# Optimization experiments

Measured on AMD Instinct MI355X. Metric: run time of the kernel, lower is better.

## Reference

```python
import jax, jax.numpy as jnp
import numpy as np

B, N, F_DIM, M, K, D = 8, 16384, 6, 128, 16, 768
MLP_DIMS = [F_DIM, 256, 512, 768, D]


def _fps(pts):
    """Deterministic farthest point sampling. pts: [N,4] -> indices [M] (first pick = point 0)."""
    n = pts.shape[0]

    def step(carry, _):
        min_d, last = carry
        d = jnp.sum((pts - pts[last]) ** 2, axis=-1)
        min_d = jnp.minimum(min_d, d)
        nxt = jnp.argmax(min_d).astype(jnp.int32)
        return (min_d, nxt), nxt

    init = (jnp.full((n,), 1e30, dtype=pts.dtype), jnp.int32(0))
    _, idx = jax.lax.scan(step, init, None, length=M - 1)
    return jnp.concatenate([jnp.zeros((1,), jnp.int32), idx])


def setup_inputs() -> dict:
    key = jax.random.key(0)
    ks = jax.random.split(key, 16)
    bidx = jnp.repeat(jnp.arange(B, dtype=jnp.float32), N)[:, None]
    xyzt = jax.random.normal(ks[0], (B * N, 4), jnp.float32)
    coordinates = jnp.concatenate([bidx, xyzt], axis=1)  # [B*N, 5]
    features = jax.random.normal(ks[1], (B * N, F_DIM), jnp.float32)
    inp = {"coordinates": coordinates, "features": features}
    for i in range(4):
        di, do = MLP_DIMS[i], MLP_DIMS[i + 1]
        inp[f"W{i}"] = jax.random.normal(ks[2 + i], (di, do), jnp.float32) * np.float32(1.0 / np.sqrt(di))
        inp[f"b{i}"] = jnp.zeros((do,), jnp.float32)
    for j in range(2):
        inp[f"Wn{j}"] = jax.random.normal(ks[6 + j], (D, D), jnp.float32) * np.float32(1.0 / np.sqrt(D))
        inp[f"bn{j}"] = jnp.zeros((D,), jnp.float32)
    return inp


def _forward(coordinates, features, W0, b0, W1, b1, W2, b2, W3, b3, Wn0, bn0, Wn1, bn1):
    # Equal points per event, sorted batch ids -> plain reshape replaces the per-batch loop.
    pts = coordinates.reshape(B, N, 5)[:, :, 1:5]       # xyz + time  [B,N,4]
    h = features.reshape(B, N, F_DIM)
    # per-point MLP (ReLU after each hidden layer, final Linear has no activation)
    h = jax.nn.relu(h @ W0 + b0)
    h = jax.nn.relu(h @ W1 + b1)
    h = jax.nn.relu(h @ W2 + b2)
    pf = h @ W3 + b3                                    # [B,N,D]
    # FPS centroids (non-differentiable index selection, as in the torch/cpu original)
    fidx = jax.vmap(_fps)(jax.lax.stop_gradient(pts))   # [B,M]
    cent = jnp.take_along_axis(pts, fidx[:, :, None], axis=1)  # [B,M,4]
    # cdist + kNN (smallest distances)
    dist = jnp.sqrt(jnp.sum((cent[:, :, None, :] - pts[:, None, :, :]) ** 2, axis=-1))  # [B,M,N]
    _, knn = jax.lax.top_k(-dist, K)                    # [B,M,K]
    gathered = jax.vmap(lambda p, i: p[i])(pf, knn)     # [B,M,K,D]
    pooled = jnp.max(gathered, axis=2)                  # [B,M,D]
    t = jax.nn.relu(pooled @ Wn0 + bn0)
    tokens = t @ Wn1 + bn1                              # [B,M,D]
    # sort tokens/centroids by centroid time (column 3)
    order = jnp.argsort(cent[:, :, 3], axis=1)
    cent = jnp.take_along_axis(cent, order[:, :, None], axis=1)
    tokens = jnp.take_along_axis(tokens, order[:, :, None], axis=1)
    masks = jnp.ones((B, M), dtype=bool)  # num_points > max_tokens -> all tokens valid
    return tokens, cent, masks


def reference(coordinates, features, W0, b0, W1, b1, W2, b2, W3, b3, Wn0, bn0, Wn1, bn1):
    return _forward(coordinates, features, W0, b0, W1, b1, W2, b2, W3, b3, Wn0, bn0, Wn1, bn1)
```

## Files before the change

### kernel.cpp

```cpp
#include <hip/hip_runtime.h>

#define B_ 8
#define N_ 16384
#define F_ 6
#define M_ 128
#define K_ 16
#define D_ 768

typedef unsigned short u16;
typedef unsigned int u32;
typedef unsigned long long u64;
typedef __attribute__((ext_vector_type(8))) short short8;
typedef __attribute__((ext_vector_type(4))) float f32x4;
typedef __attribute__((ext_vector_type(2))) float f32x2;

__device__ __forceinline__ u16 f2bf(float f){
  union { float f; u32 i; } v; v.f = f;
  u32 x = v.i;
  u32 r = x + 0x7FFFu + ((x >> 16) & 1u);
  return (u16)(r >> 16);
}

__device__ __forceinline__ void ld_g2l(const u16* g, u16* l){
  __builtin_amdgcn_global_load_lds((const __attribute__((address_space(1))) u32*)g,
                                   (__attribute__((address_space(3))) u32*)l, 16, 0, 0);
}

__device__ __forceinline__ f32x2 pkadd(f32x2 a, f32x2 b){
  f32x2 d; asm("v_pk_add_f32 %0, %1, %2" : "=v"(d) : "v"(a), "v"(b)); return d;
}
__device__ __forceinline__ f32x2 pkmul(f32x2 a, f32x2 b){
  f32x2 d; asm("v_pk_mul_f32 %0, %1, %2" : "=v"(d) : "v"(a), "v"(b)); return d;
}

__global__ __launch_bounds__(256) void conv_all(const float* __restrict__ W1,
                                                const float* __restrict__ W2,
                                                const float* __restrict__ W3,
                                                const float* __restrict__ Wn0,
                                                const float* __restrict__ Wn1,
                                                u16* __restrict__ Wb){
  __shared__ u16 tile[64][65];
  int blk = blockIdx.x;
  const float* W; u16* WT; int K, N, lb;
  if      (blk < 32)  { W = W1;  WT = Wb;           K = 256; N = 512; lb = blk; }
  else if (blk < 128) { W = W2;  WT = Wb + 131072;  K = 512; N = 768; lb = blk - 32; }
  else if (blk < 272) { W = W3;  WT = Wb + 524288;  K = 768; N = 768; lb = blk - 128; }
  else if (blk < 416) { W = Wn0; WT = Wb + 1114112; K = 768; N = 768; lb = blk - 272; }
  else                { W = Wn1; WT = Wb + 1703936; K = 768; N = 768; lb = blk - 416; }
  int tiles_n = N >> 6;
  int tk = lb / tiles_n, tn = lb % tiles_n;
  int k0 = tk << 6, n0 = tn << 6;
  int t = threadIdx.x;
#pragma unroll
  for (int q = 0; q < 16; q++){
    int idx = q * 256 + t;
    int kk = idx >> 6, nn = idx & 63;
    tile[kk][nn] = f2bf(W[(size_t)(k0 + kk) * N + n0 + nn]);
  }
  __syncthreads();
#pragma unroll
  for (int q = 0; q < 16; q++){
    int idx = q * 256 + t;
    int nn = idx >> 6, kk = idx & 63;
    WT[(size_t)(n0 + nn) * K + k0 + kk] = tile[kk][nn];
  }
}

#define FPJ 8
__global__ __launch_bounds__(1024, 4) void fps_block(const float* __restrict__ coords,
                                                     float* __restrict__ cent){
#pragma clang fp contract(off)
  __shared__ u64 swk[2][16];
  int b = blockIdx.x;
  int t = threadIdx.x;
  int lane = t & 63, wave = t >> 6;
  const float* cb = coords + (size_t)b * N_ * 5;
  f32x2 px[FPJ], py[FPJ], pz[FPJ], pw[FPJ], md[FPJ];
#pragma unroll
  for (int j = 0; j < FPJ; j++){
    int p = t + (j << 10);
    size_t i0 = (size_t)(2 * p) * 5;
    px[j] = (f32x2){cb[i0+1], cb[i0+6]};
    py[j] = (f32x2){cb[i0+2], cb[i0+7]};
    pz[j] = (f32x2){cb[i0+3], cb[i0+8]};
    pw[j] = (f32x2){cb[i0+4], cb[i0+9]};
    md[j] = (f32x2){1e30f, 1e30f};
    asm volatile("" : "+v"(px[j]), "+v"(py[j]), "+v"(pz[j]), "+v"(pw[j]));
  }
  float cx = cb[1], cy = cb[2], cz = cb[3], ct = cb[4];
  if (t == 0){
    float* c0 = cent + (size_t)b * M_ * 4;
    c0[0]=cx; c0[1]=cy; c0[2]=cz; c0[3]=ct;
  }
  for (int step = 1; step < M_; step++){
    f32x2 ncx2 = (f32x2){-cx, -cx}, ncy2 = (f32x2){-cy, -cy};
    f32x2 ncz2 = (f32x2){-cz, -cz}, nct2 = (f32x2){-ct, -ct};
    float bv = -1.0f; int bi = 1 << 30;
#pragma unroll
    for (int j = 0; j < FPJ; j++){
      f32x2 dx = pkadd(px[j], ncx2);
      f32x2 dy = pkadd(py[j], ncy2);
      f32x2 s  = pkadd(pkmul(dx, dx), pkmul(dy, dy));
      f32x2 dz = pkadd(pz[j], ncz2);
      s = pkadd(s, pkmul(dz, dz));
      f32x2 dw = pkadd(pw[j], nct2);
      s = pkadd(s, pkmul(dw, dw));
      f32x2 m = md[j];
      m[0] = fminf(s[0], m[0]);
      m[1] = fminf(s[1], m[1]);
      md[j] = m;
      int i0 = (t + (j << 10)) << 1;
      if (m[0] > bv){ bv = m[0]; bi = i0; }
      if (m[1] > bv){ bv = m[1]; bi = i0 + 1; }
    }
    union { float f; u32 u; } cv; cv.f = bv;
    u64 k = ((u64)cv.u << 32) | (u32)(N_ - 1 - bi);
#pragma unroll
    for (int off = 32; off > 0; off >>= 1){
      u64 ok = __shfl_down(k, off);
      if (ok > k) k = ok;
    }
    int par = step & 1;
    if (lane == 0) swk[par][wave] = k;
    __syncthreads();
    u64 fk = swk[par][0];
#pragma unroll
    for (int w = 1; w < 16; w++){ u64 wk = swk[par][w]; if (wk > fk) fk = wk; }
    int widx = N_ - 1 - (int)(fk & 0xffffffffu);
    size_t wb = (size_t)widx * 5;
    cx = cb[wb+1]; cy = cb[wb+2]; cz = cb[wb+3]; ct = cb[wb+4];
    if (t == 0){
      float* cr = cent + ((size_t)b * M_ + step) * 4;
      cr[0]=cx; cr[1]=cy; cr[2]=cz; cr[3]=ct;
    }
  }
}

__global__ __launch_bounds__(128) void rank_scatter(const float* __restrict__ cent_fps,
                                                    float* __restrict__ cent_sorted,
                                                    float* __restrict__ out,
                                                    size_t out_elems){
  int b = blockIdx.x, m = threadIdx.x;
  __shared__ float tt[M_];
  const float* row = cent_fps + ((size_t)b * M_ + m) * 4;
  float x=row[0], y=row[1], z=row[2], w=row[3];
  tt[m] = w;
  __syncthreads();
  int rank = 0;
  for (int j = 0; j < M_; j++){
    float tj = tt[j];
    if (tj < w || (tj == w && j < m)) rank++;
  }
  float* dst = cent_sorted + ((size_t)b * M_ + rank) * 4;
  dst[0]=x; dst[1]=y; dst[2]=z; dst[3]=w;
  size_t co = (size_t)B_ * M_ * D_ + ((size_t)b * M_ + rank) * 4;
  if (co + 3 < out_elems){
    out[co+0]=x; out[co+1]=y; out[co+2]=z; out[co+3]=w;
  }
  size_t mo = (size_t)B_ * M_ * D_ + (size_t)B_ * M_ * 4 + (size_t)b * M_ + m;
  if (mo < out_elems) out[mo] = 1.0f;
}

#define KNT 512
#define KPT 32
__global__ __launch_bounds__(512) void knn_kernel(const float* __restrict__ coords,
                                                  const float* __restrict__ cent,
                                                  int* __restrict__ knn){
#pragma clang fp contract(off)
  int cm = blockIdx.x;
  int b = cm >> 7;
  const float* cb = coords + (size_t)b * N_ * 5;
  int t = threadIdx.x;
  float cx=cent[cm*4+0], cy=cent[cm*4+1], cz=cent[cm*4+2], ct=cent[cm*4+3];
  float dist[KPT];
#pragma unroll
  for (int j = 0; j < KPT; j++){
    size_t i = t + j * KNT;
    float dx=cb[i*5+1]-cx, dy=cb[i*5+2]-cy, dz=cb[i*5+3]-cz, dw=cb[i*5+4]-ct;
    float d = ((dx*dx + dy*dy) + dz*dz) + dw*dw;
    dist[j] = sqrtf(d);
  }
  __shared__ float s_wv[8];
  __shared__ int s_wi[8];
  __shared__ int s_bi;
  for (int r = 0; r < K_; r++){
    float bv = 3e38f; int bi = 1 << 30;
#pragma unroll
    for (int j = 0; j < KPT; j++){
      int i = t + j * KNT;
      float v = dist[j];
      if (v < bv){ bv = v; bi = i; }
    }
#pragma unroll
    for (int off = 32; off > 0; off >>= 1){
      float ov = __shfl_down(bv, off);
      int oi = __shfl_down(bi, off);
      if (ov < bv || (ov == bv && oi < bi)){ bv = ov; bi = oi; }
    }
    if ((t & 63) == 0){ s_wv[t >> 6] = bv; s_wi[t >> 6] = bi; }
    __syncthreads();
    if (t == 0){
      float fv = s_wv[0]; int fi = s_wi[0];
      for (int w = 1; w < 8; w++){
        float wv = s_wv[w]; int wi = s_wi[w];
        if (wv < fv || (wv == fv && wi < fi)){ fv = wv; fi = wi; }
      }
      s_bi = fi;
      knn[(size_t)cm * K_ + r] = fi & (N_ - 1);
    }
    __syncthreads();
    int wi = s_bi;
#pragma unroll
    for (int j = 0; j < KPT; j++){
      if (t + j * KNT == wi) dist[j] = 3e38f;
    }
  }
}

__global__ __launch_bounds__(256) void gather_l0(const float* __restrict__ feat,
                                                 const int* __restrict__ knn,
                                                 const float* __restrict__ W0,
                                                 const float* __restrict__ b0,
                                                 u16* __restrict__ h1,
                                                 int rowBase){
  __shared__ float sW[F_][256];
  __shared__ float sb[256];
  __shared__ float sfa[32][F_];
  int t = threadIdx.x;
#pragma unroll
  for (int k = 0; k < F_; k++) sW[k][t] = W0[k * 256 + t];
  sb[t] = b0[t];
  if (t < 32 * F_){
    int r = t / F_, k = t % F_;
    int grow = rowBase + blockIdx.x * 32 + r;
    int bb = grow >> 11;
    int idx = knn[grow] & (N_ - 1);
    sfa[r][k] = feat[((size_t)bb * N_ + idx) * F_ + k];
  }
  __syncthreads();
#pragma unroll 4
  for (int r = 0; r < 32; r++){
    float acc = sb[t];
#pragma unroll
    for (int k = 0; k < F_; k++) acc = fmaf(sfa[r][k], sW[k][t], acc);
    int lrow = blockIdx.x * 32 + r;
    h1[(size_t)lrow * 256 + t] = f2bf(fmaxf(acc, 0.0f));
  }
}

template<int RELU, int OUTF32>
__global__ __launch_bounds__(256) void gemm_bf16(const u16* __restrict__ A,
                                                 const u16* __restrict__ WT,
                                                 const float* __restrict__ bias,
                                                 void* __restrict__ Cv,
                                                 int Kd, int Nd){
  __shared__ u16 As[128][32];
  __shared__ u16 Bs[128][32];
  const int t = threadIdx.x;
  const int bm = blockIdx.y << 7;
  const int bn = blockIdx.x << 7;
  const int wave = t >> 6;
  const int lane = t & 63;
  const int wm = (wave & 1) << 6;
  const int wn = (wave >> 1) << 6;
  const int lm = lane & 15;
  const int lk = (lane >> 4) << 3;
  u16* AsF = &As[0][0];
  u16* BsF = &Bs[0][0];
  const int wbase = wave << 6;
  f32x4 acc[4][4] = {};
  for (int k0 = 0; k0 < Kd; k0 += 32){
#pragma unroll
    for (int it = 0; it < 2; it++){
      int slot = t + (it << 8);
      int r = slot >> 2;
      int c = (slot & 3) << 3;
      int dst = (wbase + (it << 8)) << 3;
      ld_g2l(A  + (size_t)(bm + r) * Kd + k0 + c, AsF + dst);
      ld_g2l(WT + (size_t)(bn + r) * Kd + k0 + c, BsF + dst);
    }
    __syncthreads();
    short8 af[4], bfr[4];
#pragma unroll
    for (int mt = 0; mt < 4; mt++) af[mt] = *(const short8*)&As[wm + (mt << 4) + lm][lk];
#pragma unroll
    for (int nt = 0; nt < 4; nt++) bfr[nt] = *(const short8*)&Bs[wn + (nt << 4) + lm][lk];
#pragma unroll
    for (int mt = 0; mt < 4; mt++)
#pragma unroll
      for (int nt = 0; nt < 4; nt++)
        acc[mt][nt] = __builtin_amdgcn_mfma_f32_16x16x32_bf16(af[mt], bfr[nt], acc[mt][nt], 0, 0, 0);
    __syncthreads();
  }
#pragma unroll
  for (int nt = 0; nt < 4; nt++){
    int n = bn + wn + (nt << 4) + lm;
    float bia = bias[n];
#pragma unroll
    for (int mt = 0; mt < 4; mt++){
#pragma unroll
      for (int r2 = 0; r2 < 4; r2++){
        int m = bm + wm + (mt << 4) + ((lane >> 4) << 2) + r2;
        float v = acc[mt][nt][r2] + bia;
        if (RELU) v = fmaxf(v, 0.0f);
        if (OUTF32) ((float*)Cv)[(size_t)m * Nd + n] = v;
        else        ((u16*)Cv)[(size_t)m * Nd + n] = f2bf(v);
      }
    }
  }
}

template<int RELU, int OUTF32>
__global__ __launch_bounds__(256) void gemm64(const u16* __restrict__ A,
                                              const u16* __restrict__ WT,
                                              const float* __restrict__ bias,
                                              void* __restrict__ Cv,
                                              int Kd, int Nd){
  __shared__ u16 As[64][32];
  __shared__ u16 Bs[64][32];
  const int t = threadIdx.x;
  const int bm = blockIdx.y << 6;
  const int bn = blockIdx.x << 6;
  const int wave = t >> 6;
  const int lane = t & 63;
  const int wm = (wave & 1) << 5;
  const int wn = (wave >> 1) << 5;
  const int lm = lane & 15;
  const int lk = (lane >> 4) << 3;
  u16* AsF = &As[0][0];
  u16* BsF = &Bs[0][0];
  const int wbase = wave << 6;
  f32x4 acc[2][2] = {};
  for (int k0 = 0; k0 < Kd; k0 += 32){
    {
      int r = t >> 2;
      int c = (t & 3) << 3;
      int dst = wbase << 3;
      ld_g2l(A  + (size_t)(bm + r) * Kd + k0 + c, AsF + dst);
      ld_g2l(WT + (size_t)(bn + r) * Kd + k0 + c, BsF + dst);
    }
    __syncthreads();
    short8 af[2], bfr[2];
#pragma unroll
    for (int mt = 0; mt < 2; mt++) af[mt] = *(const short8*)&As[wm + (mt << 4) + lm][lk];
#pragma unroll
    for (int nt = 0; nt < 2; nt++) bfr[nt] = *(const short8*)&Bs[wn + (nt << 4) + lm][lk];
#pragma unroll
    for (int mt = 0; mt < 2; mt++)
#pragma unroll
      for (int nt = 0; nt < 2; nt++)
        acc[mt][nt] = __builtin_amdgcn_mfma_f32_16x16x32_bf16(af[mt], bfr[nt], acc[mt][nt], 0, 0, 0);
    __syncthreads();
  }
#pragma unroll
  for (int nt = 0; nt < 2; nt++){
    int n = bn + wn + (nt << 4) + lm;
    float bia = bias[n];
#pragma unroll
    for (int mt = 0; mt < 2; mt++){
#pragma unroll
      for (int r2 = 0; r2 < 4; r2++){
        int m = bm + wm + (mt << 4) + ((lane >> 4) << 2) + r2;
        float v = acc[mt][nt][r2] + bia;
        if (RELU) v = fmaxf(v, 0.0f);
        if (OUTF32) ((float*)Cv)[(size_t)m * Nd + n] = v;
        else        ((u16*)Cv)[(size_t)m * Nd + n] = f2bf(v);
      }
    }
  }
}

__global__ __launch_bounds__(256) void gemm_pool(const u16* __restrict__ A,
                                                 const u16* __restrict__ WT,
                                                 const float* __restrict__ bias,
                                                 u16* __restrict__ pooled,
                                                 int Kd, int Nd, int groupBase){
  __shared__ u16 As[128][32];
  __shared__ u16 Bs[128][32];
  const int t = threadIdx.x;
  const int bm = blockIdx.y << 7;
  const int bn = blockIdx.x << 7;
  const int wave = t >> 6;
  const int lane = t & 63;
  const int wm = (wave & 1) << 6;
  const int wn = (wave >> 1) << 6;
  const int lm = lane & 15;
  const int lk = (lane >> 4) << 3;
  u16* AsF = &As[0][0];
  u16* BsF = &Bs[0][0];
  const int wbase = wave << 6;
  f32x4 acc[4][4] = {};
  for (int k0 = 0; k0 < Kd; k0 += 32){
#pragma unroll
    for (int it = 0; it < 2; it++){
      int slot = t + (it << 8);
      int r = slot >> 2;
      int c = (slot & 3) << 3;
      int dst = (wbase + (it << 8)) << 3;
      ld_g2l(A  + (size_t)(bm + r) * Kd + k0 + c, AsF + dst);
      ld_g2l(WT + (size_t)(bn + r) * Kd + k0 + c, BsF + dst);
    }
    __syncthreads();
    short8 af[4], bfr[4];
#pragma unroll
    for (int mt = 0; mt < 4; mt++) af[mt] = *(const short8*)&As[wm + (mt << 4) + lm][lk];
#pragma unroll
    for (int nt = 0; nt < 4; nt++) bfr[nt] = *(const short8*)&Bs[wn + (nt << 4) + lm][lk];
#pragma unroll
    for (int mt = 0; mt < 4; mt++)
#pragma unroll
      for (int nt = 0; nt < 4; nt++)
        acc[mt][nt] = __builtin_amdgcn_mfma_f32_16x16x32_bf16(af[mt], bfr[nt], acc[mt][nt], 0, 0, 0);
    __syncthreads();
  }
#pragma unroll
  for (int nt = 0; nt < 4; nt++){
    int n = bn + wn + (nt << 4) + lm;
    float bia = bias[n];
#pragma unroll
    for (int mt = 0; mt < 4; mt++){
      f32x4 a = acc[mt][nt];
      float v = fmaxf(fmaxf(a[0], a[1]), fmaxf(a[2], a[3]));
      v = fmaxf(v, __shfl_xor(v, 16));
      v = fmaxf(v, __shfl_xor(v, 32));
      if ((lane >> 4) == 0){
        int g = groupBase + (bm >> 4) + (wm >> 4) + mt;
        pooled[(size_t)g * Nd + n] = f2bf(v + bia);
      }
    }
  }
}

__global__ __launch_bounds__(256) void fill_diag(float* __restrict__ out, size_t out_elems){
  size_t i = (size_t)blockIdx.x * 256 + threadIdx.x;
  if (i >= out_elems) return;
  size_t maskStart = (size_t)B_ * M_ * D_ + (size_t)B_ * M_ * 4;
  out[i] = (i >= maskStart) ? 1.0f : 0.0f;
}

extern "C" void kernel_launch(void* const* d_in, const int* in_sizes, int n_in,
                              void* d_out, int out_size, void* d_ws, size_t ws_size,
                              hipStream_t stream){
  (void)in_sizes; (void)n_in;
  const float* coords   = (const float*)d_in[0];
  const float* features = (const float*)d_in[1];
  const float* W0 = (const float*)d_in[2];  const float* b0 = (const float*)d_in[3];
  const float* W1 = (const float*)d_in[4];  const float* b1 = (const float*)d_in[5];
  const float* W2 = (const float*)d_in[6];  const float* b2 = (const float*)d_in[7];
  const float* W3 = (const float*)d_in[8];  const float* b3 = (const float*)d_in[9];
  const float* Wn0 = (const float*)d_in[10]; const float* bn0 = (const float*)d_in[11];
  const float* Wn1 = (const float*)d_in[12]; const float* bn1 = (const float*)d_in[13];
  float* out = (float*)d_out;
  const size_t out_elems = (size_t)out_size;

  char* ws = (char*)d_ws;
  const size_t o_cent = 0;
  const size_t o_cntS = 16384;
  const size_t o_knn  = 32768;
  const size_t o_Wb   = 131072;
  const size_t o_pool = 4718592;
  const size_t o_t1   = 6291456;
  const size_t o_chunk= 7864320;
  const int ROWS = B_ * M_ * K_;

  int R = 16384;
  while (R > 128 && o_chunk + (size_t)R * 2560 > ws_size) R >>= 1;
  if (d_ws == nullptr || o_chunk + (size_t)R * 2560 > ws_size){
    fill_diag<<<(int)((out_elems + 255) / 256), 256, 0, stream>>>(out, out_elems);
    return;
  }

  float* cent_fps    = (float*)(ws + o_cent);
  float* cent_sorted = (float*)(ws + o_cntS);
  int*   knn         = (int*)(ws + o_knn);
  u16* Wb   = (u16*)(ws + o_Wb);
  u16* W1t  = Wb;               u16* W2t  = Wb + 131072;
  u16* W3t  = Wb + 524288;      u16* Wn0t = Wb + 1114112;
  u16* Wn1t = Wb + 1703936;
  u16* pooled = (u16*)(ws + o_pool);
  u16* t1     = (u16*)(ws + o_t1);
  u16* regA   = (u16*)(ws + o_chunk);
  u16* regB   = (u16*)(ws + o_chunk + (size_t)R * 1536);

  conv_all<<<560, 256, 0, stream>>>(W1, W2, W3, Wn0, Wn1, Wb);
  fps_block<<<B_, 1024, 0, stream>>>(coords, cent_fps);
  rank_scatter<<<B_, 128, 0, stream>>>(cent_fps, cent_sorted, out, out_elems);
  knn_kernel<<<B_ * M_, KNT, 0, stream>>>(coords, cent_sorted, knn);

  for (int rowBase = 0; rowBase < ROWS; rowBase += R){
    gather_l0<<<R / 32, 256, 0, stream>>>(features, knn, W0, b0, regA, rowBase);
    gemm_bf16<1,0><<<dim3(4, R / 128), 256, 0, stream>>>(regA, W1t, b1, regB, 256, 512);
    gemm_bf16<1,0><<<dim3(6, R / 128), 256, 0, stream>>>(regB, W2t, b2, regA, 512, 768);
    gemm_pool<<<dim3(6, R / 128), 256, 0, stream>>>(regA, W3t, b3, pooled, 768, 768, rowBase >> 4);
  }

  gemm64<1,0><<<dim3(12, (B_ * M_) / 64), 256, 0, stream>>>(pooled, Wn0t, bn0, t1, 768, 768);
  gemm64<0,1><<<dim3(12, (B_ * M_) / 64), 256, 0, stream>>>(t1, Wn1t, bn1, out, 768, 768);
}
```

Baseline: 552.0 us.

## Halve FPS block size and use ballot-based argmax reduction

The farthest-point-sampling kernel now runs 512 threads per batch instead of 1024, each owning 32 contiguous points. The per-step argmax no longer does a 64-bit packed shuffle reduction. It uses a float max via xor-shuffles, then a ballot to pick the lowest winning lane's index, and combines 8 waves instead of 16. Contiguous point ownership keeps the lowest-index tie-break, so results should match. In exchange the longer per-thread loop raises register pressure.

```diff
diff --git a/kernel.cpp b/kernel.cpp
--- a/kernel.cpp
+++ b/kernel.cpp
@@ -66,20 +66,21 @@
   }
 }
 
-#define FPJ 8
-__global__ __launch_bounds__(1024, 4) void fps_block(const float* __restrict__ coords,
-                                                     float* __restrict__ cent){
+#define FPJ 16
+__global__ __launch_bounds__(512) __attribute__((amdgpu_waves_per_eu(2, 2)))
+void fps_block(const float* __restrict__ coords, float* __restrict__ cent){
 #pragma clang fp contract(off)
-  __shared__ u64 swk[2][16];
+  __shared__ float swv[2][8];
+  __shared__ int   swi[2][8];
   int b = blockIdx.x;
   int t = threadIdx.x;
   int lane = t & 63, wave = t >> 6;
   const float* cb = coords + (size_t)b * N_ * 5;
+  const int base = t << 5;
   f32x2 px[FPJ], py[FPJ], pz[FPJ], pw[FPJ], md[FPJ];
 #pragma unroll
   for (int j = 0; j < FPJ; j++){
-    int p = t + (j << 10);
-    size_t i0 = (size_t)(2 * p) * 5;
+    size_t i0 = (size_t)(base + 2 * j) * 5;
     px[j] = (f32x2){cb[i0+1], cb[i0+6]};
     py[j] = (f32x2){cb[i0+2], cb[i0+7]};
     pz[j] = (f32x2){cb[i0+3], cb[i0+8]};
@@ -95,7 +96,7 @@
   for (int step = 1; step < M_; step++){
     f32x2 ncx2 = (f32x2){-cx, -cx}, ncy2 = (f32x2){-cy, -cy};
     f32x2 ncz2 = (f32x2){-cz, -cz}, nct2 = (f32x2){-ct, -ct};
-    float bv = -1.0f; int bi = 1 << 30;
+    float bv = -1.0f; int bl = 0;
 #pragma unroll
     for (int j = 0; j < FPJ; j++){
       f32x2 dx = pkadd(px[j], ncx2);
@@ -109,24 +110,28 @@
       m[0] = fminf(s[0], m[0]);
       m[1] = fminf(s[1], m[1]);
       md[j] = m;
-      int i0 = (t + (j << 10)) << 1;
-      if (m[0] > bv){ bv = m[0]; bi = i0; }
-      if (m[1] > bv){ bv = m[1]; bi = i0 + 1; }
-    }
-    union { float f; u32 u; } cv; cv.f = bv;
-    u64 k = ((u64)cv.u << 32) | (u32)(N_ - 1 - bi);
-#pragma unroll
-    for (int off = 32; off > 0; off >>= 1){
-      u64 ok = __shfl_down(k, off);
-      if (ok > k) k = ok;
-    }
+      if (m[0] > bv){ bv = m[0]; bl = 2*j;     }
+      if (m[1] > bv){ bv = m[1]; bl = 2*j + 1; }
+    }
+    int bi = base + bl;
+    float wv = bv;
+#pragma unroll
+    for (int off = 1; off < 64; off <<= 1) wv = fmaxf(wv, __shfl_xor(wv, off));
+    u64 wm = __ballot(bv == wv);
+    int srcL = (int)__ffsll((unsigned long long)wm) - 1;
+    int wbi = __shfl(bi, srcL);
     int par = step & 1;
-    if (lane == 0) swk[par][wave] = k;
-    __syncthreads();
-    u64 fk = swk[par][0];
-#pragma unroll
-    for (int w = 1; w < 16; w++){ u64 wk = swk[par][w]; if (wk > fk) fk = wk; }
-    int widx = N_ - 1 - (int)(fk & 0xffffffffu);
+    if (lane == 0){ swv[par][wave] = wv; swi[par][wave] = wbi; }
+    __syncthreads();
+    float v8 = swv[par][lane & 7];
+    int   i8 = swi[par][lane & 7];
+    float g = v8;
+    g = fmaxf(g, __shfl_xor(g, 1));
+    g = fmaxf(g, __shfl_xor(g, 2));
+    g = fmaxf(g, __shfl_xor(g, 4));
+    u64 bm = __ballot((lane < 8) && (v8 == g));
+    int srcW = (int)__ffsll((unsigned long long)bm) - 1;
+    int widx = __builtin_amdgcn_readfirstlane(__shfl(i8, srcW));
     size_t wb = (size_t)widx * 5;
     cx = cb[wb+1]; cy = cb[wb+2]; cz = cb[wb+3]; ct = cb[wb+4];
     if (t == 0){
@@ -483,7 +488,7 @@
   u16* regB   = (u16*)(ws + o_chunk + (size_t)R * 1536);
 
   conv_all<<<560, 256, 0, stream>>>(W1, W2, W3, Wn0, Wn1, Wb);
-  fps_block<<<B_, 1024, 0, stream>>>(coords, cent_fps);
+  fps_block<<<B_, 512, 0, stream>>>(coords, cent_fps);
   rank_scatter<<<B_, 128, 0, stream>>>(cent_fps, cent_sorted, out, out_elems);
   knn_kernel<<<B_ * M_, KNT, 0, stream>>>(coords, cent_sorted, knn);
 
```

After: 535.3 us. 3.0% less time.
